# Kernel optimization log

Measured on AMD Instinct MI355X. Metric: run time of the kernel, lower is better.

## Reference

```python
import jax, jax.numpy as jnp
import numpy as np

N, n, m, k = 100000, 32, 16, 32
MU = 100.0  # bubble kernel scale (init arg mu)


def setup_inputs() -> dict:
    key = jax.random.key(0)
    ks = jax.random.split(key, 7)
    x = jax.random.normal(ks[0], (N,), dtype=jnp.float32)
    # torch.nn.Linear(N, n): weight [n, N], bias [n]
    encoder_w = jax.random.normal(ks[1], (n, N), dtype=jnp.float32) / np.float32(np.sqrt(N))
    encoder_b = jnp.zeros((n,), dtype=jnp.float32)
    # decoder parameter [n, N]
    decoder = jax.random.normal(ks[2], (n, N), dtype=jnp.float32) / np.float32(np.sqrt(n))
    # torch.nn.Linear(n, n*m): weight [n*m, n], bias [n*m]
    bw_w = jax.random.normal(ks[3], (n * m, n), dtype=jnp.float32) / np.float32(np.sqrt(n))
    bw_b = jnp.zeros((n * m,), dtype=jnp.float32)
    neighbour_distance = jax.random.uniform(ks[4], (N, k), dtype=jnp.float32)
    neighbour_id = jax.random.randint(ks[5], (N, k), 0, N)
    clustering_labels = jax.random.randint(ks[6], (N,), 0, m)
    return {
        "x": x,
        "encoder_w": encoder_w,
        "encoder_b": encoder_b,
        "decoder": decoder,
        "bw_w": bw_w,
        "bw_b": bw_b,
        "neighbour_distance": neighbour_distance,
        "neighbour_id": neighbour_id,
        "clustering_labels": clustering_labels,
    }


def reference(x, encoder_w, encoder_b, decoder, bw_w, bw_b,
              neighbour_distance, neighbour_id, clustering_labels):
    # encode: [N] -> [n]
    encoded = x @ encoder_w.T + encoder_b
    # per-basis, per-cluster bandwidths: sigmoid(Linear)/60 -> [n, m] -> expand to [n, N]
    bandwidths = jax.nn.sigmoid(encoded @ bw_w.T + bw_b) / 60.0
    w = bandwidths.reshape(n, m)[:, clustering_labels]  # [n, N]
    # bubble window: relu(1 - d^2 / (w*mu)^2) -> [n, N, k]
    window = jax.nn.relu(1.0 - neighbour_distance[None, :, :] ** 2
                         / (w[:, :, None] * MU) ** 2)
    # normalization over axis 1 (the N axis), faithful to the source's dim=1
    window = window / jnp.sum(window, axis=1, keepdims=True)
    # gather decoder rows at neighbours, weight, reduce over k: [n, N]
    convolved_basis = jnp.sum(decoder[:, neighbour_id] * window, axis=-1)
    # [n] @ [n, N] -> [N]
    return encoded @ convolved_basis
```

## Files before the change

kernel.cpp:

```cpp
#include <hip/hip_runtime.h>
#include <hip/hip_fp16.h>

#define N_PTS 100000
#define MU_F  100.0f

typedef unsigned int uint;
typedef _Float16 h2 __attribute__((ext_vector_type(2)));

#define E_SCALE 16384.0f
#define E_SCALE_INV (1.0f / 16384.0f)

#define ENC_BLKS 256
#define TR_BLKS  1563
#define HIST_BLKS 64

__global__ __launch_bounds__(256) void k_prep(const float* __restrict__ x,
                                              const float* __restrict__ encW,
                                              const float* __restrict__ encB,
                                              const float* __restrict__ dec,
                                              const int* __restrict__ labels,
                                              float* __restrict__ enc,
                                              __half* __restrict__ decT,
                                              int* __restrict__ ghist) {
    int b = blockIdx.x;
    if (b < ENC_BLKS) {
        int row = b & 31;
        int chunk = b >> 5;
        const int CH = N_PTS / 8;
        int base = chunk * CH;
        const float4* W4 = reinterpret_cast<const float4*>(encW + (size_t)row * N_PTS + base);
        const float4* x4 = reinterpret_cast<const float4*>(x + base);
        const int nv = CH / 4;
        float acc = 0.f;
        for (int idx = threadIdx.x; idx < nv; idx += 256) {
            float4 w = W4[idx];
            float4 xv = x4[idx];
            acc += w.x * xv.x + w.y * xv.y + w.z * xv.z + w.w * xv.w;
        }
        #pragma unroll
        for (int off = 32; off > 0; off >>= 1) acc += __shfl_down(acc, off);
        __shared__ float sred[4];
        int wid = threadIdx.x >> 6;
        if ((threadIdx.x & 63) == 0) sred[wid] = acc;
        __syncthreads();
        if (threadIdx.x == 0) {
            float s = sred[0] + sred[1] + sred[2] + sred[3];
            if (chunk == 0) s += encB[row];
            atomicAdd(enc + row, s);
        }
    } else if (b < ENC_BLKS + TR_BLKS) {
        __shared__ float tile[32][65];
        int j0 = (b - ENC_BLKS) * 64;
        int col = threadIdx.x & 63;
        int r0 = threadIdx.x >> 6;
        #pragma unroll
        for (int it = 0; it < 8; ++it) {
            int row = it * 4 + r0;
            int j = j0 + col;
            float v = (j < N_PTS) ? dec[(size_t)row * N_PTS + j] : 0.f;
            tile[row][col] = v;
        }
        __syncthreads();
        #pragma unroll
        for (int it = 0; it < 4; ++it) {
            int idx = it * 256 + threadIdx.x;
            int j = idx >> 4;
            int p = idx & 15;
            int jj = j0 + j;
            if (jj < N_PTS) {
                __half2 h = __halves2half2(__float2half(tile[2 * p][j]),
                                           __float2half(tile[2 * p + 1][j]));
                *reinterpret_cast<__half2*>(decT + (size_t)jj * 32 + 2 * p) = h;
            }
        }
    } else {
        __shared__ int lh[16];
        if (threadIdx.x < 16) lh[threadIdx.x] = 0;
        __syncthreads();
        int hb = b - (ENC_BLKS + TR_BLKS);
        for (int j = hb * 256 + threadIdx.x; j < N_PTS; j += HIST_BLKS * 256)
            atomicAdd(&lh[labels[j]], 1);
        __syncthreads();
        if (threadIdx.x < 16) atomicAdd(&ghist[threadIdx.x], lh[threadIdx.x]);
    }
}

__global__ __launch_bounds__(256) void k_scatter(const int* __restrict__ labels,
                                                 const int* __restrict__ ghist,
                                                 int* __restrict__ gcursor,
                                                 int* __restrict__ perm) {
    __shared__ int lh[16], lbase[16], lcur[16], gb[16];
    const int CHUNK = 784;
    int start = blockIdx.x * CHUNK;
    int end = min(start + CHUNK, N_PTS);
    if (threadIdx.x < 16) { lh[threadIdx.x] = 0; lcur[threadIdx.x] = 0; }
    if (threadIdx.x == 0) {
        int run = 0;
        for (int c = 0; c < 16; ++c) { gb[c] = run; run += ghist[c]; }
    }
    __syncthreads();
    for (int j = start + threadIdx.x; j < end; j += 256)
        atomicAdd(&lh[labels[j]], 1);
    __syncthreads();
    if (threadIdx.x < 16)
        lbase[threadIdx.x] = gb[threadIdx.x] + atomicAdd(&gcursor[threadIdx.x], lh[threadIdx.x]);
    __syncthreads();
    for (int j = start + threadIdx.x; j < end; j += 256) {
        int c = labels[j];
        int lpos = atomicAdd(&lcur[c], 1);
        perm[lbase[c] + lpos] = j;
    }
}

__device__ inline void build_invC(const float* __restrict__ encL,
                                  const float* __restrict__ bw_w,
                                  const float* __restrict__ bw_b,
                                  float* __restrict__ invCL, int c) {
    if (threadIdx.x < 32) {
        int r = threadIdx.x * 16 + c;
        float z = bw_b[r];
        const float* wr = bw_w + r * 32;
        #pragma unroll
        for (int p = 0; p < 32; ++p) z = fmaf(encL[p], wr[p], z);
        float s = 1.f / (1.f + __expf(-z));
        float wmu = s * (MU_F / 60.0f);
        invCL[threadIdx.x] = 1.f / (wmu * wmu);
    }
}

__global__ __launch_bounds__(256, 4) void k_S_sorted(const float* __restrict__ enc_g,
                                                     const float* __restrict__ bw_w,
                                                     const float* __restrict__ bw_b,
                                                     const float* __restrict__ nd,
                                                     const int* __restrict__ perm,
                                                     const int* __restrict__ ghist,
                                                     float* __restrict__ S,
                                                     float* __restrict__ S_part) {
    __shared__ float encL[32], invCL[32];
    __shared__ float Sloc[1024];
    __shared__ int baseSh[17];
    int b = blockIdx.x;
    int c = b & 15;
    int ch = b >> 4;
    if (threadIdx.x < 32) encL[threadIdx.x] = enc_g[threadIdx.x];
    for (int t = threadIdx.x; t < 1024; t += 256) Sloc[t] = 0.f;
    if (threadIdx.x == 0) {
        int run = 0;
        for (int cc = 0; cc < 16; ++cc) { baseSh[cc] = run; run += ghist[cc]; }
        baseSh[16] = run;
    }
    __syncthreads();
    build_invC(encL, bw_w, bw_b, invCL, c);
    __syncthreads();

    float invC[32];
    #pragma unroll
    for (int i = 0; i < 32; ++i) invC[i] = invCL[i];

    int bs = baseSh[c];
    int cnt = baseSh[c + 1] - bs;
    int lane = threadIdx.x & 63;
    int kk = lane & 31;
    int jh = lane >> 5;
    int gw = ch * 4 + (threadIdx.x >> 6);
    const int nw = 64 * 4;
    int npairs = (cnt + 1) >> 1;

    float acc[32];
    #pragma unroll
    for (int i = 0; i < 32; ++i) acc[i] = 0.f;

    for (int pp = gw; pp < npairs; pp += nw) {
        bool valid = (2 * pp + jh) < cnt;
        int p = valid ? (bs + 2 * pp + jh) : bs;
        int j = __builtin_nontemporal_load(&perm[p]);
        float d = __builtin_nontemporal_load(&nd[(size_t)j * 32 + kk]);
        float d2 = valid ? d * d : 1e30f;
        #pragma unroll
        for (int i = 0; i < 32; ++i)
            acc[i] += fmaxf(fmaf(-d2, invC[i], 1.0f), 0.f);
    }
    #pragma unroll
    for (int i = 0; i < 32; ++i) acc[i] += __shfl_xor(acc[i], 32);
    if (jh == 0) {
        #pragma unroll
        for (int i = 0; i < 32; ++i) atomicAdd(&Sloc[i * 32 + kk], acc[i]);
    }
    __syncthreads();
    if (S_part) {
        for (int t = threadIdx.x; t < 1024; t += 256)
            S_part[(size_t)b * 1024 + t] = Sloc[t];
    } else {
        for (int t = threadIdx.x; t < 1024; t += 256) {
            float v = Sloc[t];
            if (v != 0.f) atomicAdd(&S[t], v);
        }
    }
}

__global__ __launch_bounds__(1024) void k_S_reduce(const float* __restrict__ S_part,
                                                   float* __restrict__ S) {
    int g = blockIdx.x;
    int t = threadIdx.x;
    float s = 0.f;
    #pragma unroll
    for (int u = 0; u < 16; ++u)
        s += S_part[(size_t)(g * 16 + u) * 1024 + t];
    atomicAdd(&S[t], s);
}

__global__ __launch_bounds__(256, 6) void k_main(const float* __restrict__ enc_g,
                                                 const float* __restrict__ bw_w,
                                                 const float* __restrict__ bw_b,
                                                 const float* __restrict__ S_g,
                                                 const float* __restrict__ nd,
                                                 const int* __restrict__ nid,
                                                 const int* __restrict__ perm,
                                                 const int* __restrict__ ghist,
                                                 const __half* __restrict__ decT,
                                                 float* __restrict__ out) {
    __shared__ float encL[32], invCL[32];
    __shared__ float ELf[1024];
    __shared__ int baseSh[17];
    int c = blockIdx.x & 15;
    int ch = blockIdx.x >> 4;
    if (threadIdx.x < 32) encL[threadIdx.x] = enc_g[threadIdx.x];
    if (threadIdx.x == 0) {
        int run = 0;
        for (int cc = 0; cc < 16; ++cc) { baseSh[cc] = run; run += ghist[cc]; }
        baseSh[16] = run;
    }
    __syncthreads();
    build_invC(encL, bw_w, bw_b, invCL, c);
    for (int t = threadIdx.x; t < 1024; t += 256)
        ELf[t] = encL[t >> 5] / S_g[t] * E_SCALE;
    __syncthreads();

    int lane = threadIdx.x & 63;
    int R = lane >> 2;
    int q = lane & 3;

    float invq[8];
    h2 EhA[4], EhB[4];
    #pragma unroll
    for (int t = 0; t < 8; ++t) invq[t] = invCL[q * 8 + t];
    #pragma unroll
    for (int t = 0; t < 4; ++t) {
        int i0 = q * 8 + 2 * t, i1 = i0 + 1;
        EhA[t] = __builtin_bit_cast(h2, __builtin_amdgcn_cvt_pkrtz(
                     ELf[i0 * 32 + R], ELf[i1 * 32 + R]));
        EhB[t] = __builtin_bit_cast(h2, __builtin_amdgcn_cvt_pkrtz(
                     ELf[i0 * 32 + R + 16], ELf[i1 * 32 + R + 16]));
    }

    int bs = baseSh[c];
    int cnt = baseSh[c + 1] - bs;
    int wv = ch * 4 + (threadIdx.x >> 6);
    const int nw = 96 * 4;
    int npairs = (cnt + 1) >> 1;
    const uint4* decQ = reinterpret_cast<const uint4*>(decT);

    if (wv >= npairs) return;

    auto load_pair = [&](int pp, int& j0, int& j1, bool& v1) {
        bool ok = pp < npairs;
        int p0 = ok ? (bs + 2 * pp) : bs;
        v1 = ok && ((2 * pp + 1) < cnt);
        j0 = perm[p0];
        j1 = perm[v1 ? p0 + 1 : p0];
    };
    auto load_ids = [&](int j0, int j1, int* id, float* dd) {
        #pragma unroll
        for (int s = 0; s < 4; ++s) {
            int jj = (s >> 1) ? j1 : j0;
            size_t idx = (size_t)jj * 32 + (s & 1) * 16 + R;
            id[s] = __builtin_nontemporal_load(&nid[idx]);
            dd[s] = __builtin_nontemporal_load(&nd[idx]);
        }
    };

    int pp = wv;
    int j0a, j1a, j0b, j1b; bool v1a, v1b;
    int ida[4]; float dda[4];
    load_pair(pp, j0a, j1a, v1a);
    load_ids(j0a, j1a, ida, dda);
    load_pair(pp + nw, j0b, j1b, v1b);

    while (pp < npairs) {
        uint4 r0 = decQ[(size_t)ida[0] * 4 + q];
        uint4 r1 = decQ[(size_t)ida[1] * 4 + q];
        uint4 r2 = decQ[(size_t)ida[2] * 4 + q];
        uint4 r3 = decQ[(size_t)ida[3] * 4 + q];
        int idb[4]; float ddb[4];
        load_ids(j0b, j1b, idb, ddb);
        int j0c, j1c; bool v1c;
        load_pair(pp + 2 * nw, j0c, j1c, v1c);

        float d20 = dda[0] * dda[0];
        float d21 = dda[1] * dda[1];
        float d22 = dda[2] * dda[2];
        float d23 = dda[3] * dda[3];

        float a0 = 0.f, a1 = 0.f, a2 = 0.f, a3 = 0.f;
        #pragma unroll
        for (int t = 0; t < 4; ++t) {
            uint dw0 = (t == 0) ? r0.x : (t == 1) ? r0.y : (t == 2) ? r0.z : r0.w;
            uint dw1 = (t == 0) ? r1.x : (t == 1) ? r1.y : (t == 2) ? r1.z : r1.w;
            uint dw2 = (t == 0) ? r2.x : (t == 1) ? r2.y : (t == 2) ? r2.z : r2.w;
            uint dw3 = (t == 0) ? r3.x : (t == 1) ? r3.y : (t == 2) ? r3.z : r3.w;
            float i0v = invq[2 * t], i1v = invq[2 * t + 1];
            {
                float w0 = fmaxf(fmaf(-d20, i0v, 1.f), 0.f);
                float w1 = fmaxf(fmaf(-d20, i1v, 1.f), 0.f);
                h2 wh = __builtin_bit_cast(h2, __builtin_amdgcn_cvt_pkrtz(w0, w1));
                a0 = __builtin_amdgcn_fdot2(wh * EhA[t], __builtin_bit_cast(h2, dw0), a0, false);
            }
            {
                float w0 = fmaxf(fmaf(-d21, i0v, 1.f), 0.f);
                float w1 = fmaxf(fmaf(-d21, i1v, 1.f), 0.f);
                h2 wh = __builtin_bit_cast(h2, __builtin_amdgcn_cvt_pkrtz(w0, w1));
                a1 = __builtin_amdgcn_fdot2(wh * EhB[t], __builtin_bit_cast(h2, dw1), a1, false);
            }
            {
                float w0 = fmaxf(fmaf(-d22, i0v, 1.f), 0.f);
                float w1 = fmaxf(fmaf(-d22, i1v, 1.f), 0.f);
                h2 wh = __builtin_bit_cast(h2, __builtin_amdgcn_cvt_pkrtz(w0, w1));
                a2 = __builtin_amdgcn_fdot2(wh * EhA[t], __builtin_bit_cast(h2, dw2), a2, false);
            }
            {
                float w0 = fmaxf(fmaf(-d23, i0v, 1.f), 0.f);
                float w1 = fmaxf(fmaf(-d23, i1v, 1.f), 0.f);
                h2 wh = __builtin_bit_cast(h2, __builtin_amdgcn_cvt_pkrtz(w0, w1));
                a3 = __builtin_amdgcn_fdot2(wh * EhB[t], __builtin_bit_cast(h2, dw3), a3, false);
            }
        }
        float u = a0 + a1;
        float v = a2 + a3;
        #pragma unroll
        for (int off = 32; off > 0; off >>= 1) {
            u += __shfl_xor(u, off);
            v += __shfl_xor(v, off);
        }
        if (lane == 0) out[j0a] = u * E_SCALE_INV;
        if (lane == 32 && v1a) out[j1a] = v * E_SCALE_INV;

        j0a = j0b; j1a = j1b; v1a = v1b;
        j0b = j0c; j1b = j1c; v1b = v1c;
        #pragma unroll
        for (int s = 0; s < 4; ++s) { ida[s] = idb[s]; dda[s] = ddb[s]; }
        pp += nw;
    }
}

extern "C" void kernel_launch(void* const* d_in, const int* in_sizes, int n_in,
                              void* d_out, int out_size, void* d_ws, size_t ws_size,
                              hipStream_t stream) {
    const float* x     = (const float*)d_in[0];
    const float* enc_w = (const float*)d_in[1];
    const float* enc_b = (const float*)d_in[2];
    const float* dec   = (const float*)d_in[3];
    const float* bw_w  = (const float*)d_in[4];
    const float* bw_b  = (const float*)d_in[5];
    const float* nd    = (const float*)d_in[6];
    const int*   nid   = (const int*)d_in[7];
    const int*   labels= (const int*)d_in[8];
    float* out = (float*)d_out;

    char* ws = (char*)d_ws;
    float* enc    = (float*)(ws + 0);
    float* S      = (float*)(ws + 128);
    int* ghist    = (int*)(ws + 4224);
    int* gcursor  = (int*)(ws + 4288);
    int* perm     = (int*)(ws + 8192);
    __half* decT  = (__half*)(ws + 408576);
    bool use_part = ws_size >= 11005952ull;
    float* S_part = use_part ? (float*)(ws + 6811648) : nullptr;

    (void)hipMemsetAsync(d_ws, 0, 4352, stream);
    k_prep<<<dim3(ENC_BLKS + TR_BLKS + HIST_BLKS), dim3(256), 0, stream>>>(
        x, enc_w, enc_b, dec, labels, enc, decT, ghist);
    k_scatter<<<dim3(128), dim3(256), 0, stream>>>(labels, ghist, gcursor, perm);
    k_S_sorted<<<dim3(1024), dim3(256), 0, stream>>>(enc, bw_w, bw_b, nd, perm,
                                                     ghist, S, S_part);
    if (use_part)
        k_S_reduce<<<dim3(64), dim3(1024), 0, stream>>>(S_part, S);
    k_main<<<dim3(1536), dim3(256), 0, stream>>>(enc, bw_w, bw_b, S, nd, nid,
                                                 perm, ghist, decT, out);
}
```

Baseline: 187.3 us.

## Split decoder gather into two half-width passes and fuse scatter into prep

```diff
diff --git a/kernel.cpp b/kernel.cpp
--- a/kernel.cpp
+++ b/kernel.cpp
@@ -3,6 +3,7 @@
 
 #define N_PTS 100000
 #define MU_F  100.0f
+#define BUCKET 8192
 
 typedef unsigned int uint;
 typedef _Float16 h2 __attribute__((ext_vector_type(2)));
@@ -12,7 +13,7 @@
 
 #define ENC_BLKS 256
 #define TR_BLKS  1563
-#define HIST_BLKS 64
+#define SC_BLKS  98
 
 __global__ __launch_bounds__(256) void k_prep(const float* __restrict__ x,
                                               const float* __restrict__ encW,
@@ -20,8 +21,10 @@
                                               const float* __restrict__ dec,
                                               const int* __restrict__ labels,
                                               float* __restrict__ enc,
-                                              __half* __restrict__ decT,
-                                              int* __restrict__ ghist) {
+                                              __half* __restrict__ decT0,
+                                              __half* __restrict__ decT1,
+                                              int* __restrict__ gcur,
+                                              int* __restrict__ perm) {
     int b = blockIdx.x;
     if (b < ENC_BLKS) {
         int row = b & 31;
@@ -70,45 +73,31 @@
             if (jj < N_PTS) {
                 __half2 h = __halves2half2(__float2half(tile[2 * p][j]),
                                            __float2half(tile[2 * p + 1][j]));
-                *reinterpret_cast<__half2*>(decT + (size_t)jj * 32 + 2 * p) = h;
+                if (p < 8)
+                    *reinterpret_cast<__half2*>(decT0 + (size_t)jj * 16 + 2 * p) = h;
+                else
+                    *reinterpret_cast<__half2*>(decT1 + (size_t)jj * 16 + 2 * (p - 8)) = h;
             }
         }
     } else {
-        __shared__ int lh[16];
-        if (threadIdx.x < 16) lh[threadIdx.x] = 0;
-        __syncthreads();
-        int hb = b - (ENC_BLKS + TR_BLKS);
-        for (int j = hb * 256 + threadIdx.x; j < N_PTS; j += HIST_BLKS * 256)
+        __shared__ int lh[16], lbase[16], lcur[16];
+        const int CHUNK = 1024;
+        int start = (b - ENC_BLKS - TR_BLKS) * CHUNK;
+        int end = min(start + CHUNK, N_PTS);
+        if (threadIdx.x < 16) { lh[threadIdx.x] = 0; lcur[threadIdx.x] = 0; }
+        __syncthreads();
+        for (int j = start + threadIdx.x; j < end; j += 256)
             atomicAdd(&lh[labels[j]], 1);
         __syncthreads();
-        if (threadIdx.x < 16) atomicAdd(&ghist[threadIdx.x], lh[threadIdx.x]);
-    }
-}
-
-__global__ __launch_bounds__(256) void k_scatter(const int* __restrict__ labels,
-                                                 const int* __restrict__ ghist,
-                                                 int* __restrict__ gcursor,
-                                                 int* __restrict__ perm) {
-    __shared__ int lh[16], lbase[16], lcur[16], gb[16];
-    const int CHUNK = 784;
-    int start = blockIdx.x * CHUNK;
-    int end = min(start + CHUNK, N_PTS);
-    if (threadIdx.x < 16) { lh[threadIdx.x] = 0; lcur[threadIdx.x] = 0; }
-    if (threadIdx.x == 0) {
-        int run = 0;
-        for (int c = 0; c < 16; ++c) { gb[c] = run; run += ghist[c]; }
-    }
-    __syncthreads();
-    for (int j = start + threadIdx.x; j < end; j += 256)
-        atomicAdd(&lh[labels[j]], 1);
-    __syncthreads();
-    if (threadIdx.x < 16)
-        lbase[threadIdx.x] = gb[threadIdx.x] + atomicAdd(&gcursor[threadIdx.x], lh[threadIdx.x]);
-    __syncthreads();
-    for (int j = start + threadIdx.x; j < end; j += 256) {
-        int c = labels[j];
-        int lpos = atomicAdd(&lcur[c], 1);
-        perm[lbase[c] + lpos] = j;
+        if (threadIdx.x < 16)
+            lbase[threadIdx.x] = threadIdx.x * BUCKET +
+                                 atomicAdd(&gcur[threadIdx.x], lh[threadIdx.x]);
+        __syncthreads();
+        for (int j = start + threadIdx.x; j < end; j += 256) {
+            int c = labels[j];
+            int lpos = atomicAdd(&lcur[c], 1);
+            perm[lbase[c] + lpos] = j;
+        }
     }
 }
 
@@ -133,22 +122,16 @@
                                                      const float* __restrict__ bw_b,
                                                      const float* __restrict__ nd,
                                                      const int* __restrict__ perm,
-                                                     const int* __restrict__ ghist,
+                                                     const int* __restrict__ gcur,
                                                      float* __restrict__ S,
                                                      float* __restrict__ S_part) {
     __shared__ float encL[32], invCL[32];
     __shared__ float Sloc[1024];
-    __shared__ int baseSh[17];
     int b = blockIdx.x;
     int c = b & 15;
     int ch = b >> 4;
     if (threadIdx.x < 32) encL[threadIdx.x] = enc_g[threadIdx.x];
     for (int t = threadIdx.x; t < 1024; t += 256) Sloc[t] = 0.f;
-    if (threadIdx.x == 0) {
-        int run = 0;
-        for (int cc = 0; cc < 16; ++cc) { baseSh[cc] = run; run += ghist[cc]; }
-        baseSh[16] = run;
-    }
     __syncthreads();
     build_invC(encL, bw_w, bw_b, invCL, c);
     __syncthreads();
@@ -157,8 +140,8 @@
     #pragma unroll
     for (int i = 0; i < 32; ++i) invC[i] = invCL[i];
 
-    int bs = baseSh[c];
-    int cnt = baseSh[c + 1] - bs;
+    int bs = c * BUCKET;
+    int cnt = gcur[c];
     int lane = threadIdx.x & 63;
     int kk = lane & 31;
     int jh = lane >> 5;
@@ -170,15 +153,27 @@
     #pragma unroll
     for (int i = 0; i < 32; ++i) acc[i] = 0.f;
 
-    for (int pp = gw; pp < npairs; pp += nw) {
+    if (gw < npairs) {
+        int pp = gw;
         bool valid = (2 * pp + jh) < cnt;
         int p = valid ? (bs + 2 * pp + jh) : bs;
         int j = __builtin_nontemporal_load(&perm[p]);
         float d = __builtin_nontemporal_load(&nd[(size_t)j * 32 + kk]);
-        float d2 = valid ? d * d : 1e30f;
-        #pragma unroll
-        for (int i = 0; i < 32; ++i)
-            acc[i] += fmaxf(fmaf(-d2, invC[i], 1.0f), 0.f);
+        while (pp < npairs) {
+            int pn = pp + nw;
+            bool vn = false; float dn = 0.f;
+            if (pn < npairs) {
+                vn = (2 * pn + jh) < cnt;
+                int p2 = vn ? (bs + 2 * pn + jh) : bs;
+                int jn = __builtin_nontemporal_load(&perm[p2]);
+                dn = __builtin_nontemporal_load(&nd[(size_t)jn * 32 + kk]);
+            }
+            float d2 = valid ? d * d : 1e30f;
+            #pragma unroll
+            for (int i = 0; i < 32; ++i)
+                acc[i] += fmaxf(fmaf(-d2, invC[i], 1.0f), 0.f);
+            d = dn; valid = vn; pp = pn;
+        }
     }
     #pragma unroll
     for (int i = 0; i < 32; ++i) acc[i] += __shfl_xor(acc[i], 32);
@@ -209,27 +204,23 @@
     atomicAdd(&S[t], s);
 }
 
-__global__ __launch_bounds__(256, 6) void k_main(const float* __restrict__ enc_g,
+__global__ __launch_bounds__(256, 4) void k_main(const float* __restrict__ enc_g,
                                                  const float* __restrict__ bw_w,
                                                  const float* __restrict__ bw_b,
                                                  const float* __restrict__ S_g,
                                                  const float* __restrict__ nd,
                                                  const int* __restrict__ nid,
                                                  const int* __restrict__ perm,
-                                                 const int* __restrict__ ghist,
-                                                 const __half* __restrict__ decT,
-                                                 float* __restrict__ out) {
+                                                 const int* __restrict__ gcur,
+                                                 const __half* __restrict__ decT0,
+                                                 const __half* __restrict__ decT1,
+                                                 float* __restrict__ out,
+                                                 float* __restrict__ out2) {
     __shared__ float encL[32], invCL[32];
     __shared__ float ELf[1024];
-    __shared__ int baseSh[17];
     int c = blockIdx.x & 15;
     int ch = blockIdx.x >> 4;
     if (threadIdx.x < 32) encL[threadIdx.x] = enc_g[threadIdx.x];
-    if (threadIdx.x == 0) {
-        int run = 0;
-        for (int cc = 0; cc < 16; ++cc) { baseSh[cc] = run; run += ghist[cc]; }
-        baseSh[16] = run;
-    }
     __syncthreads();
     build_invC(encL, bw_w, bw_b, invCL, c);
     for (int t = threadIdx.x; t < 1024; t += 256)
@@ -237,29 +228,30 @@
     __syncthreads();
 
     int lane = threadIdx.x & 63;
-    int R = lane >> 2;
-    int q = lane & 3;
-
-    float invq[8];
-    h2 EhA[4], EhB[4];
-    #pragma unroll
-    for (int t = 0; t < 8; ++t) invq[t] = invCL[q * 8 + t];
+    int R = lane >> 1;
+    int q = lane & 1;
+
+    float invA[8], invB[8];
+    h2 EA[4], EB[4];
+    #pragma unroll
+    for (int t = 0; t < 8; ++t) {
+        invA[t] = invCL[q * 8 + t];
+        invB[t] = invCL[16 + q * 8 + t];
+    }
     #pragma unroll
     for (int t = 0; t < 4; ++t) {
-        int i0 = q * 8 + 2 * t, i1 = i0 + 1;
-        EhA[t] = __builtin_bit_cast(h2, __builtin_amdgcn_cvt_pkrtz(
-                     ELf[i0 * 32 + R], ELf[i1 * 32 + R]));
-        EhB[t] = __builtin_bit_cast(h2, __builtin_amdgcn_cvt_pkrtz(
-                     ELf[i0 * 32 + R + 16], ELf[i1 * 32 + R + 16]));
-    }
-
-    int bs = baseSh[c];
-    int cnt = baseSh[c + 1] - bs;
+        int i0 = q * 8 + 2 * t;
+        EA[t] = __builtin_bit_cast(h2, __builtin_amdgcn_cvt_pkrtz(
+                    ELf[i0 * 32 + R], ELf[(i0 + 1) * 32 + R]));
+        EB[t] = __builtin_bit_cast(h2, __builtin_amdgcn_cvt_pkrtz(
+                    ELf[(16 + i0) * 32 + R], ELf[(16 + i0 + 1) * 32 + R]));
+    }
+
+    int bs = c * BUCKET;
+    int cnt = gcur[c];
     int wv = ch * 4 + (threadIdx.x >> 6);
-    const int nw = 96 * 4;
+    const int nw = 64 * 4;
     int npairs = (cnt + 1) >> 1;
-    const uint4* decQ = reinterpret_cast<const uint4*>(decT);
-
     if (wv >= npairs) return;
 
     auto load_pair = [&](int pp, int& j0, int& j1, bool& v1) {
@@ -269,87 +261,76 @@
         j0 = perm[p0];
         j1 = perm[v1 ? p0 + 1 : p0];
     };
-    auto load_ids = [&](int j0, int j1, int* id, float* dd) {
-        #pragma unroll
-        for (int s = 0; s < 4; ++s) {
-            int jj = (s >> 1) ? j1 : j0;
-            size_t idx = (size_t)jj * 32 + (s & 1) * 16 + R;
-            id[s] = __builtin_nontemporal_load(&nid[idx]);
-            dd[s] = __builtin_nontemporal_load(&nd[idx]);
-        }
+    auto load_ids = [&](int j0, int j1, int& i0, int& i1, float& d0, float& d1) {
+        size_t x0 = (size_t)j0 * 32 + R;
+        size_t x1 = (size_t)j1 * 32 + R;
+        i0 = __builtin_nontemporal_load(&nid[x0]);
+        d0 = __builtin_nontemporal_load(&nd[x0]);
+        i1 = __builtin_nontemporal_load(&nid[x1]);
+        d1 = __builtin_nontemporal_load(&nd[x1]);
     };
 
-    int pp = wv;
-    int j0a, j1a, j0b, j1b; bool v1a, v1b;
-    int ida[4]; float dda[4];
-    load_pair(pp, j0a, j1a, v1a);
-    load_ids(j0a, j1a, ida, dda);
-    load_pair(pp + nw, j0b, j1b, v1b);
-
-    while (pp < npairs) {
-        uint4 r0 = decQ[(size_t)ida[0] * 4 + q];
-        uint4 r1 = decQ[(size_t)ida[1] * 4 + q];
-        uint4 r2 = decQ[(size_t)ida[2] * 4 + q];
-        uint4 r3 = decQ[(size_t)ida[3] * 4 + q];
-        int idb[4]; float ddb[4];
-        load_ids(j0b, j1b, idb, ddb);
-        int j0c, j1c; bool v1c;
-        load_pair(pp + 2 * nw, j0c, j1c, v1c);
-
-        float d20 = dda[0] * dda[0];
-        float d21 = dda[1] * dda[1];
-        float d22 = dda[2] * dda[2];
-        float d23 = dda[3] * dda[3];
-
-        float a0 = 0.f, a1 = 0.f, a2 = 0.f, a3 = 0.f;
-        #pragma unroll
-        for (int t = 0; t < 4; ++t) {
-            uint dw0 = (t == 0) ? r0.x : (t == 1) ? r0.y : (t == 2) ? r0.z : r0.w;
-            uint dw1 = (t == 0) ? r1.x : (t == 1) ? r1.y : (t == 2) ? r1.z : r1.w;
-            uint dw2 = (t == 0) ? r2.x : (t == 1) ? r2.y : (t == 2) ? r2.z : r2.w;
-            uint dw3 = (t == 0) ? r3.x : (t == 1) ? r3.y : (t == 2) ? r3.z : r3.w;
-            float i0v = invq[2 * t], i1v = invq[2 * t + 1];
-            {
-                float w0 = fmaxf(fmaf(-d20, i0v, 1.f), 0.f);
-                float w1 = fmaxf(fmaf(-d20, i1v, 1.f), 0.f);
-                h2 wh = __builtin_bit_cast(h2, __builtin_amdgcn_cvt_pkrtz(w0, w1));
-                a0 = __builtin_amdgcn_fdot2(wh * EhA[t], __builtin_bit_cast(h2, dw0), a0, false);
+    auto run_half = [&](const uint4* __restrict__ decQ,
+                        const float* inv, const h2* E,
+                        float* __restrict__ ob) {
+        int pp = wv;
+        int j0a, j1a, j0b, j1b; bool v1a, v1b;
+        int ida0, ida1; float dda0, dda1;
+        load_pair(pp, j0a, j1a, v1a);
+        load_ids(j0a, j1a, ida0, ida1, dda0, dda1);
+        load_pair(pp + nw, j0b, j1b, v1b);
+        while (pp < npairs) {
+            uint4 r0 = decQ[(size_t)ida0 * 2 + q];
+            uint4 r1 = decQ[(size_t)ida1 * 2 + q];
+            int idb0, idb1; float ddb0, ddb1;
+            load_ids(j0b, j1b, idb0, idb1, ddb0, ddb1);
+            int j0c, j1c; bool v1c;
+            load_pair(pp + 2 * nw, j0c, j1c, v1c);
+
+            float d20 = dda0 * dda0;
+            float d21 = dda1 * dda1;
+            float a0 = 0.f, a1 = 0.f;
+            #pragma unroll
+            for (int t = 0; t < 4; ++t) {
+                uint dw0 = (t == 0) ? r0.x : (t == 1) ? r0.y : (t == 2) ? r0.z : r0.w;
+                uint dw1 = (t == 0) ? r1.x : (t == 1) ? r1.y : (t == 2) ? r1.z : r1.w;
+                float i0v = inv[2 * t], i1v = inv[2 * t + 1];
+                {
+                    float w0 = fmaxf(fmaf(-d20, i0v, 1.f), 0.f);
+                    float w1 = fmaxf(fmaf(-d20, i1v, 1.f), 0.f);
+                    h2 wh = __builtin_bit_cast(h2, __builtin_amdgcn_cvt_pkrtz(w0, w1));
+                    a0 = __builtin_amdgcn_fdot2(wh * E[t], __builtin_bit_cast(h2, dw0), a0, false);
+                }
+                {
+                    float w0 = fmaxf(fmaf(-d21, i0v, 1.f), 0.f);
+                    float w1 = fmaxf(fmaf(-d21, i1v, 1.f), 0.f);
+                    h2 wh = __builtin_bit_cast(h2, __builtin_amdgcn_cvt_pkrtz(w0, w1));
+                    a1 = __builtin_amdgcn_fdot2(wh * E[t], __builtin_bit_cast(h2, dw1), a1, false);
+                }
             }
-            {
-                float w0 = fmaxf(fmaf(-d21, i0v, 1.f), 0.f);
-                float w1 = fmaxf(fmaf(-d21, i1v, 1.f), 0.f);
-                h2 wh = __builtin_bit_cast(h2, __builtin_amdgcn_cvt_pkrtz(w0, w1));
-                a1 = __builtin_amdgcn_fdot2(wh * EhB[t], __builtin_bit_cast(h2, dw1), a1, false);
+            #pragma unroll
+            for (int off = 32; off > 0; off >>= 1) {
+                a0 += __shfl_xor(a0, off);
+                a1 += __shfl_xor(a1, off);
             }
-            {
-                float w0 = fmaxf(fmaf(-d22, i0v, 1.f), 0.f);
-                float w1 = fmaxf(fmaf(-d22, i1v, 1.f), 0.f);
-                h2 wh = __builtin_bit_cast(h2, __builtin_amdgcn_cvt_pkrtz(w0, w1));
-                a2 = __builtin_amdgcn_fdot2(wh * EhA[t], __builtin_bit_cast(h2, dw2), a2, false);
-            }
-            {
-                float w0 = fmaxf(fmaf(-d23, i0v, 1.f), 0.f);
-                float w1 = fmaxf(fmaf(-d23, i1v, 1.f), 0.f);
-                h2 wh = __builtin_bit_cast(h2, __builtin_amdgcn_cvt_pkrtz(w0, w1));
-                a3 = __builtin_amdgcn_fdot2(wh * EhB[t], __builtin_bit_cast(h2, dw3), a3, false);
-            }
-        }
-        float u = a0 + a1;
-        float v = a2 + a3;
-        #pragma unroll
-        for (int off = 32; off > 0; off >>= 1) {
-            u += __shfl_xor(u, off);
-            v += __shfl_xor(v, off);
-        }
-        if (lane == 0) out[j0a] = u * E_SCALE_INV;
-        if (lane == 32 && v1a) out[j1a] = v * E_SCALE_INV;
-
-        j0a = j0b; j1a = j1b; v1a = v1b;
-        j0b = j0c; j1b = j1c; v1b = v1c;
-        #pragma unroll
-        for (int s = 0; s < 4; ++s) { ida[s] = idb[s]; dda[s] = ddb[s]; }
-        pp += nw;
-    }
+            if (lane == 0) ob[j0a] = a0 * E_SCALE_INV;
+            if (lane == 32 && v1a) ob[j1a] = a1 * E_SCALE_INV;
+
+            j0a = j0b; j1a = j1b; v1a = v1b;
+            j0b = j0c; j1b = j1c; v1b = v1c;
+            ida0 = idb0; ida1 = idb1; dda0 = ddb0; dda1 = ddb1;
+            pp += nw;
+        }
+    };
+
+    run_half(reinterpret_cast<const uint4*>(decT0), invA, EA, out);
+    run_half(reinterpret_cast<const uint4*>(decT1), invB, EB, out2);
+}
+
+__global__ __launch_bounds__(256) void k_add(const float* __restrict__ out2,
+                                             float* __restrict__ out) {
+    int j = blockIdx.x * 256 + threadIdx.x;
+    if (j < N_PTS) out[j] += out2[j];
 }
 
 extern "C" void kernel_launch(void* const* d_in, const int* in_sizes, int n_in,
@@ -369,21 +350,23 @@
     char* ws = (char*)d_ws;
     float* enc    = (float*)(ws + 0);
     float* S      = (float*)(ws + 128);
-    int* ghist    = (int*)(ws + 4224);
-    int* gcursor  = (int*)(ws + 4288);
+    int* gcur     = (int*)(ws + 4224);
     int* perm     = (int*)(ws + 8192);
-    __half* decT  = (__half*)(ws + 408576);
-    bool use_part = ws_size >= 11005952ull;
-    float* S_part = use_part ? (float*)(ws + 6811648) : nullptr;
-
-    (void)hipMemsetAsync(d_ws, 0, 4352, stream);
-    k_prep<<<dim3(ENC_BLKS + TR_BLKS + HIST_BLKS), dim3(256), 0, stream>>>(
-        x, enc_w, enc_b, dec, labels, enc, decT, ghist);
-    k_scatter<<<dim3(128), dim3(256), 0, stream>>>(labels, ghist, gcursor, perm);
+    __half* decT0 = (__half*)(ws + 532480);
+    __half* decT1 = (__half*)(ws + 3732480);
+    bool use_part = ws_size >= 11526784ull;
+    float* S_part = use_part ? (float*)(ws + 6932480) : nullptr;
+    float* out2   = use_part ? (float*)(ws + 11126784) : (float*)(ws + 6932480);
+
+    (void)hipMemsetAsync(d_ws, 0, 4288, stream);
+    k_prep<<<dim3(ENC_BLKS + TR_BLKS + SC_BLKS), dim3(256), 0, stream>>>(
+        x, enc_w, enc_b, dec, labels, enc, decT0, decT1, gcur, perm);
     k_S_sorted<<<dim3(1024), dim3(256), 0, stream>>>(enc, bw_w, bw_b, nd, perm,
-                                                     ghist, S, S_part);
+                                                     gcur, S, S_part);
     if (use_part)
         k_S_reduce<<<dim3(64), dim3(1024), 0, stream>>>(S_part, S);
-    k_main<<<dim3(1536), dim3(256), 0, stream>>>(enc, bw_w, bw_b, S, nd, nid,
-                                                 perm, ghist, decT, out);
-}
+    k_main<<<dim3(1024), dim3(256), 0, stream>>>(enc, bw_w, bw_b, S, nd, nid,
+                                                 perm, gcur, decT0, decT1,
+                                                 out, out2);
+    k_add<<<dim3((N_PTS + 255) / 256), dim3(256), 0, stream>>>(out2, out);
+}
```

Result: slower. 201.5 us (+7.6%).
